# Optimization experiments

Hardware: AMD Instinct MI355X
Metric: run time of the kernel (lower is better)

## Reference

```python
import jax, jax.numpy as jnp
import numpy as np

B, T, C = 4, 2048, 1024
H = 16
HS = C // H  # 64
FF = 4 * C  # 4096


def setup_inputs() -> dict:
    key = jax.random.key(0)
    ks = jax.random.split(key, 10)
    s_in = C ** -0.5
    s_ff = FF ** -0.5
    return {
        "x": jax.random.normal(ks[0], (B, T, C), dtype=jnp.float32),
        "Wq": jax.random.normal(ks[1], (H, C, HS), dtype=jnp.float32) * s_in,
        "Wk": jax.random.normal(ks[2], (H, C, HS), dtype=jnp.float32) * s_in,
        "Wv": jax.random.normal(ks[3], (H, C, HS), dtype=jnp.float32) * s_in,
        "Wproj": jax.random.normal(ks[4], (C, C), dtype=jnp.float32) * s_in,
        "bproj": jax.random.normal(ks[5], (C,), dtype=jnp.float32) * 0.01,
        "W1": jax.random.normal(ks[6], (C, FF), dtype=jnp.float32) * s_in,
        "b1": jax.random.normal(ks[7], (FF,), dtype=jnp.float32) * 0.01,
        "W2": jax.random.normal(ks[8], (FF, C), dtype=jnp.float32) * s_ff,
        "b2": jax.random.normal(ks[9], (C,), dtype=jnp.float32) * 0.01,
    }


def reference(x, Wq, Wk, Wv, Wproj, bproj, W1, b1, W2, b2):
    b, t, c = x.shape
    # per-head projections, batched over heads: [B,H,T,HS]
    q = jnp.einsum("btc,hcd->bhtd", x, Wq)
    k = jnp.einsum("btc,hcd->bhtd", x, Wk)
    v = jnp.einsum("btc,hcd->bhtd", x, Wv)
    # NOTE: original scales by full embed dim c**-0.5, not head_size
    scores = jnp.einsum("bhtd,bhsd->bhts", q, k) * (c ** -0.5)
    causal = jnp.tril(jnp.ones((t, t), dtype=bool))
    scores = jnp.where(causal[None, None], scores, -jnp.inf)
    w = jax.nn.softmax(scores, axis=-1)
    y = jnp.einsum("bhts,bhsd->bhtd", w, v)  # [B,H,T,HS]
    y = jnp.transpose(y, (0, 2, 1, 3)).reshape(b, t, c)  # concat heads
    attn_out = y @ Wproj + bproj
    x = attn_out + x
    ff = jax.nn.relu(x @ W1 + b1) @ W2 + b2
    return ff + x
```

## Files before the change

kernel.cpp:

```cpp
#include <hip/hip_runtime.h>

typedef unsigned short u16;
typedef __attribute__((ext_vector_type(4))) float f32x4;
typedef __attribute__((ext_vector_type(8))) short bf16x8;

constexpr int kB  = 4;
constexpr int kT  = 2048;
constexpr int kC  = 1024;
constexpr int kH  = 16;
constexpr int kFF = 4096;
constexpr int kM  = kB * kT;
constexpr int k3C = 3 * kC;

__device__ __forceinline__ float b2f(u16 u) {
    union { unsigned int i; float f; } v;
    v.i = ((unsigned int)u) << 16;
    return v.f;
}
__device__ __forceinline__ u16 f2b(float f) {
    union { float f; unsigned int i; } v;
    v.f = f;
    unsigned int r = (v.i + 0x7FFFu + ((v.i >> 16) & 1u)) >> 16;
    return (u16)r;
}

__device__ __forceinline__ void lds_barrier() {
    __asm__ __volatile__("" ::: "memory");
    __builtin_amdgcn_s_waitcnt(0xC07F);
    __builtin_amdgcn_s_barrier();
    __asm__ __volatile__("" ::: "memory");
}

__global__ void cvt_f32_bf16(const float* __restrict__ in, u16* __restrict__ out, int n4)
{
    const int i = blockIdx.x * 256 + threadIdx.x;
    if (i >= n4) return;
    float4 v = *(const float4*)(in + (size_t)i * 4);
    ushort4 o;
    o.x = f2b(v.x); o.y = f2b(v.y); o.z = f2b(v.z); o.w = f2b(v.w);
    *(ushort4*)(out + (size_t)i * 4) = o;
}

__global__ void transpose_cvt(const float* __restrict__ in, int R, int Cc,
                              u16* __restrict__ out)
{
    __shared__ float t[32][33];
    const int bx = blockIdx.x * 32;
    const int by = blockIdx.y * 32;
    const int lx = threadIdx.x, ly = threadIdx.y;
    #pragma unroll
    for (int i = 0; i < 32; i += 8)
        t[ly + i][lx] = in[(size_t)(by + ly + i) * Cc + bx + lx];
    __syncthreads();
    #pragma unroll
    for (int i = 0; i < 32; i += 8)
        out[(size_t)(bx + ly + i) * R + by + lx] = f2b(t[lx][ly + i]);
}

__global__ void repack_qkv_t(const float* __restrict__ Wq, const float* __restrict__ Wk,
                             const float* __restrict__ Wv, u16* __restrict__ out)
{
    __shared__ float t[32][33];
    const int z = blockIdx.z;
    const int s = z >> 4, h = z & 15;
    const float* in = (s == 0 ? Wq : s == 1 ? Wk : Wv) + (size_t)h * (kC * 64);
    const int bx = blockIdx.x * 32;
    const int by = blockIdx.y * 32;
    const int lx = threadIdx.x, ly = threadIdx.y;
    #pragma unroll
    for (int i = 0; i < 32; i += 8)
        t[ly + i][lx] = in[(size_t)(by + ly + i) * 64 + bx + lx];
    __syncthreads();
    const int orow = s * kC + h * 64 + bx;
    #pragma unroll
    for (int i = 0; i < 32; i += 8)
        out[(size_t)(orow + ly + i) * kC + by + lx] = f2b(t[lx][ly + i]);
}

__global__ __launch_bounds__(256) void gemm_bt_mfma(
    const u16* __restrict__ A, int lda,
    const u16* __restrict__ Bt, int ldb,
    int K,
    const float* __restrict__ bias,
    const u16* __restrict__ resid,
    float* __restrict__ CoF,
    u16* __restrict__ CoB,
    int ldc, int do_relu)
{
    constexpr int BK = 64;
    __shared__ u16 As[128 * BK];
    __shared__ u16 Bs[128 * BK];
    const int tid  = threadIdx.x;
    const int wave = tid >> 6, lane = tid & 63;
    const int wm = (wave >> 1) * 64, wn = (wave & 1) * 64;
    const int m0 = blockIdx.y * 128, n0 = blockIdx.x * 128;

    const int srow = wave * 32;
    const int lrow = lane >> 3;
    const int scol = ((lane & 7) ^ lrow) * 8;

    const int fm   = lane & 15;
    const int fkq  = lane >> 4;

    f32x4 acc[4][4];
    #pragma unroll
    for (int i = 0; i < 4; ++i)
        #pragma unroll
        for (int j = 0; j < 4; ++j)
            acc[i][j] = (f32x4){0.f, 0.f, 0.f, 0.f};

    for (int k0 = 0; k0 < K; k0 += BK) {
        #pragma unroll
        for (int i = 0; i < 4; ++i) {
            const int r = srow + i * 8;
            const u16* ga = A  + (size_t)(m0 + r + lrow) * lda + k0 + scol;
            const u16* gb = Bt + (size_t)(n0 + r + lrow) * ldb + k0 + scol;
            __builtin_amdgcn_global_load_lds(
                (const __attribute__((address_space(1))) void*)ga,
                (__attribute__((address_space(3))) void*)&As[r * BK], 16, 0, 0);
            __builtin_amdgcn_global_load_lds(
                (const __attribute__((address_space(1))) void*)gb,
                (__attribute__((address_space(3))) void*)&Bs[r * BK], 16, 0, 0);
        }
        __syncthreads();
        #pragma unroll
        for (int ks = 0; ks < 2; ++ks) {
            bf16x8 a[4], b[4];
            #pragma unroll
            for (int i = 0; i < 4; ++i) {
                const int m = wm + i * 16 + fm;
                const int ck = ((ks * 4 + fkq) ^ (m & 7)) * 8;
                a[i] = *(const bf16x8*)&As[m * BK + ck];
            }
            #pragma unroll
            for (int j = 0; j < 4; ++j) {
                const int n = wn + j * 16 + fm;
                const int ck = ((ks * 4 + fkq) ^ (n & 7)) * 8;
                b[j] = *(const bf16x8*)&Bs[n * BK + ck];
            }
            #pragma unroll
            for (int i = 0; i < 4; ++i)
                #pragma unroll
                for (int j = 0; j < 4; ++j)
                    acc[i][j] = __builtin_amdgcn_mfma_f32_16x16x32_bf16(
                        a[i], b[j], acc[i][j], 0, 0, 0);
        }
        __syncthreads();
    }

    const int col = lane & 15;
    const int rb  = (lane >> 4) * 4;
    #pragma unroll
    for (int i = 0; i < 4; ++i) {
        #pragma unroll
        for (int j = 0; j < 4; ++j) {
            const int n = n0 + wn + j * 16 + col;
            #pragma unroll
            for (int r = 0; r < 4; ++r) {
                const int m = m0 + wm + i * 16 + rb + r;
                float v = acc[i][j][r];
                if (bias)    v += bias[n];
                if (do_relu) v = fmaxf(v, 0.f);
                if (resid)   v += b2f(resid[(size_t)m * ldc + n]);
                if (CoF) CoF[(size_t)m * ldc + n] = v;
                else     CoB[(size_t)m * ldc + n] = f2b(v);
            }
        }
    }
}

__global__ __launch_bounds__(256) void attn_mfma3(
    const u16* __restrict__ QKV, u16* __restrict__ Y)
{
    __shared__ __align__(16) u16 Kl[2][64 * 64];
    __shared__ __align__(16) u16 Vt[2][64 * 64];
    __shared__ __align__(16) u16 Pl[4][16 * 64];

    const int tid  = threadIdx.x;
    const int wave = tid >> 6, lane = tid & 63;
    const int ln = lane & 15, quad = lane >> 4;
    const int idx = blockIdx.x;
    const int bh = idx & 63;
    const int qt = 15 - (idx >> 6);
    const int b = bh >> 4, h = bh & 15;
    const int q0 = qt << 7;
    const int bT = b * kT;
    const int qgw = q0 + wave * 32;
    const float scale = 0.03125f;

    const u16* kvbase = QKV + (size_t)bT * k3C + kC + h * 64;

    const int sK = tid >> 3, cK = tid & 7;
    const int sV = (tid >> 3) * 2, cV = tid & 7;
    const int kwa0 = (sK << 6) + ((cK ^ (sK & 7)) << 3);
    const int kwa1 = kwa0 + (32 << 6);

    bf16x8 qa[2][2];
    #pragma unroll
    for (int qsub = 0; qsub < 2; ++qsub) {
        const size_t qb = ((size_t)bT + qgw + 16 * qsub + ln) * k3C + h * 64;
        qa[qsub][0] = *(const bf16x8*)(QKV + qb + quad * 8);
        qa[qsub][1] = *(const bf16x8*)(QKV + qb + 32 + quad * 8);
    }

    f32x4 acco[2][4];
    #pragma unroll
    for (int qsub = 0; qsub < 2; ++qsub)
        #pragma unroll
        for (int jd = 0; jd < 4; ++jd) acco[qsub][jd] = (f32x4){0.f, 0.f, 0.f, 0.f};
    float mrun[2] = {-1e30f, -1e30f}, lrun[2] = {0.f, 0.f};
    u16* Pw = Pl[wave];

    const int ntiles = 2 * qt + 2;

    auto loadkv = [&](int s0p, uint4& k0, uint4& k1, uint4& v0, uint4& v1) {
        const u16* kg = kvbase + (size_t)(s0p + sK) * k3C + cK * 8;
        k0 = *(const uint4*)kg;
        k1 = *(const uint4*)(kg + (size_t)32 * k3C);
        const u16* vg = kvbase + kC + (size_t)(s0p + sV) * k3C + cV * 8;
        v0 = *(const uint4*)vg;
        v1 = *(const uint4*)(vg + k3C);
    };
    auto stage = [&](u16* Kb, u16* Vb, const uint4& k0, const uint4& k1,
                     const uint4& v0, const uint4& v1) {
        *(uint4*)&Kb[kwa0] = k0;
        *(uint4*)&Kb[kwa1] = k1;
        const u16* t0 = (const u16*)&v0;
        const u16* t1 = (const u16*)&v1;
        #pragma unroll
        for (int i = 0; i < 8; ++i) {
            const int d = cV * 8 + i;
            const int chunk = ((sV >> 3) ^ (d & 7) ^ ((d >> 3) & 7)) & 7;
            ushort2 pr; pr.x = t0[i]; pr.y = t1[i];
            *(ushort2*)&Vb[(d << 6) + (chunk << 3) + (sV & 7)] = pr;
        }
    };
    auto compute = [&](int t, const u16* Kb, const u16* Vb) {
        const int s0 = t << 6;
        if (s0 > qgw + 31) return;
        f32x4 accs[2][4];
        #pragma unroll
        for (int qsub = 0; qsub < 2; ++qsub)
            #pragma unroll
            for (int j = 0; j < 4; ++j) accs[qsub][j] = (f32x4){0.f, 0.f, 0.f, 0.f};
        #pragma unroll
        for (int ks = 0; ks < 2; ++ks) {
            #pragma unroll
            for (int j = 0; j < 4; ++j) {
                const int s = j * 16 + ln;
                bf16x8 kb = *(const bf16x8*)&Kb[(s << 6) + ((((quad + 4 * ks) ^ (s & 7)) & 7) << 3)];
                accs[0][j] = __builtin_amdgcn_mfma_f32_16x16x32_bf16(kb, qa[0][ks], accs[0][j], 0, 0, 0);
                accs[1][j] = __builtin_amdgcn_mfma_f32_16x16x32_bf16(kb, qa[1][ks], accs[1][j], 0, 0, 0);
            }
        }
        bf16x8 vfr[4][2];
        #pragma unroll
        for (int jd = 0; jd < 4; ++jd) {
            const int d = jd * 16 + ln;
            #pragma unroll
            for (int ks = 0; ks < 2; ++ks)
                vfr[jd][ks] = *(const bf16x8*)&Vb[(d << 6) + ((((quad + 4 * ks) ^ (d & 7) ^ ((d >> 3) & 7)) & 7) << 3)];
        }
        #pragma unroll
        for (int qsub = 0; qsub < 2; ++qsub) {
            const int qg = qgw + 16 * qsub + ln;
            float part = -1e30f;
            #pragma unroll
            for (int j = 0; j < 4; ++j) {
                #pragma unroll
                for (int r = 0; r < 4; ++r) {
                    const int sg = s0 + j * 16 + quad * 4 + r;
                    float v = accs[qsub][j][r] * scale;
                    v = (sg <= qg) ? v : -1e30f;
                    accs[qsub][j][r] = v;
                    part = fmaxf(part, v);
                }
            }
            float mx = fmaxf(part, __shfl_xor(part, 16));
            mx = fmaxf(mx, __shfl_xor(mx, 32));
            const float mn = fmaxf(mrun[qsub], mx);
            const float al = __expf(mrun[qsub] - mn);
            mrun[qsub] = mn;
            float ls = 0.f;
            #pragma unroll
            for (int j = 0; j < 4; ++j)
                #pragma unroll
                for (int r = 0; r < 4; ++r) {
                    const float p = __expf(accs[qsub][j][r] - mn);
                    accs[qsub][j][r] = p;
                    ls += p;
                }
            ls += __shfl_xor(ls, 16);
            ls += __shfl_xor(ls, 32);
            lrun[qsub] = lrun[qsub] * al + ls;
            #pragma unroll
            for (int jd = 0; jd < 4; ++jd)
                #pragma unroll
                for (int r = 0; r < 4; ++r)
                    acco[qsub][jd][r] *= al;
            #pragma unroll
            for (int j = 0; j < 4; ++j) {
                ushort4 pk;
                pk.x = f2b(accs[qsub][j][0]); pk.y = f2b(accs[qsub][j][1]);
                pk.z = f2b(accs[qsub][j][2]); pk.w = f2b(accs[qsub][j][3]);
                const int chunk = ((2 * j + (quad >> 1)) ^ (ln & 7)) & 7;
                *(ushort4*)&Pw[(ln << 6) + (chunk << 3) + ((quad & 1) << 2)] = pk;
            }
            #pragma unroll
            for (int ks = 0; ks < 2; ++ks) {
                bf16x8 pb = *(const bf16x8*)&Pw[(ln << 6) + ((((4 * ks + quad) ^ (ln & 7)) & 7) << 3)];
                #pragma unroll
                for (int jd = 0; jd < 4; ++jd)
                    acco[qsub][jd] = __builtin_amdgcn_mfma_f32_16x16x32_bf16(
                        vfr[jd][ks], pb, acco[qsub][jd], 0, 0, 0);
            }
        }
    };

    uint4 ka0, ka1, va0, va1, kb0, kb1, vb0, vb1;
    loadkv(0, ka0, ka1, va0, va1);
    for (int t = 0; t < ntiles; t += 2) {
        stage(Kl[0], Vt[0], ka0, ka1, va0, va1);
        loadkv((t + 1) << 6, kb0, kb1, vb0, vb1);
        lds_barrier();
        compute(t, Kl[0], Vt[0]);
        stage(Kl[1], Vt[1], kb0, kb1, vb0, vb1);
        loadkv(((t + 2) < ntiles ? (t + 2) : 0) << 6, ka0, ka1, va0, va1);
        lds_barrier();
        compute(t + 1, Kl[1], Vt[1]);
    }

    #pragma unroll
    for (int qsub = 0; qsub < 2; ++qsub) {
        const float inv = 1.f / lrun[qsub];
        const size_t yrow = ((size_t)bT + qgw + 16 * qsub + ln) * kC + h * 64;
        #pragma unroll
        for (int jd = 0; jd < 4; ++jd) {
            ushort4 ov;
            ov.x = f2b(acco[qsub][jd][0] * inv);
            ov.y = f2b(acco[qsub][jd][1] * inv);
            ov.z = f2b(acco[qsub][jd][2] * inv);
            ov.w = f2b(acco[qsub][jd][3] * inv);
            *(ushort4*)(Y + yrow + jd * 16 + quad * 4) = ov;
        }
    }
}

extern "C" void kernel_launch(void* const* d_in, const int* in_sizes, int n_in,
                              void* d_out, int out_size, void* d_ws, size_t ws_size,
                              hipStream_t stream) {
    const float* x     = (const float*)d_in[0];
    const float* Wq    = (const float*)d_in[1];
    const float* Wk    = (const float*)d_in[2];
    const float* Wv    = (const float*)d_in[3];
    const float* Wproj = (const float*)d_in[4];
    const float* bproj = (const float*)d_in[5];
    const float* W1    = (const float*)d_in[6];
    const float* b1    = (const float*)d_in[7];
    const float* W2    = (const float*)d_in[8];
    const float* b2    = (const float*)d_in[9];

    u16* ws      = (u16*)d_ws;
    u16* QKV     = ws;
    u16* ffh     = ws;
    u16* attn_y  = ws + (size_t)kM * kFF;
    u16* xb      = attn_y  + (size_t)kM * kC;
    u16* res1    = xb      + (size_t)kM * kC;
    u16* Wqkv_t  = res1    + (size_t)kM * kC;
    u16* Wproj_t = Wqkv_t  + (size_t)k3C * kC;
    u16* W1t     = Wproj_t + (size_t)kC * kC;
    u16* W2t     = W1t     + (size_t)kFF * kC;
    float* out   = (float*)d_out;

    cvt_f32_bf16<<<(kM * kC / 4 + 255) / 256, 256, 0, stream>>>(x, xb, kM * kC / 4);
    repack_qkv_t<<<dim3(2, kC / 32, 48), dim3(32, 8), 0, stream>>>(Wq, Wk, Wv, Wqkv_t);
    transpose_cvt<<<dim3(kC / 32, kC / 32),  dim3(32, 8), 0, stream>>>(Wproj, kC, kC, Wproj_t);
    transpose_cvt<<<dim3(kFF / 32, kC / 32), dim3(32, 8), 0, stream>>>(W1, kC, kFF, W1t);
    transpose_cvt<<<dim3(kC / 32, kFF / 32), dim3(32, 8), 0, stream>>>(W2, kFF, kC, W2t);

    gemm_bt_mfma<<<dim3(k3C / 128, kM / 128), 256, 0, stream>>>(
        xb, kC, Wqkv_t, kC, kC, nullptr, nullptr, nullptr, QKV, k3C, 0);
    attn_mfma3<<<dim3(1024), 256, 0, stream>>>(QKV, attn_y);
    gemm_bt_mfma<<<dim3(kC / 128, kM / 128), 256, 0, stream>>>(
        attn_y, kC, Wproj_t, kC, kC, bproj, xb, nullptr, res1, kC, 0);
    gemm_bt_mfma<<<dim3(kFF / 128, kM / 128), 256, 0, stream>>>(
        res1, kC, W1t, kC, kC, b1, nullptr, nullptr, ffh, kFF, 1);
    gemm_bt_mfma<<<dim3(kC / 128, kM / 128), 256, 0, stream>>>(
        ffh, kFF, W2t, kFF, kFF, b2, res1, out, nullptr, kC, 0);
}
```

Measured before the change: 588.0 us.

## Replace GEMM with 256x256 double-buffered ping-pong pipelined MFMA kernel

Measured after the change: 649.4 us. +10.4%, slower.

```diff
diff --git a/kernel.cpp b/kernel.cpp
--- a/kernel.cpp
+++ b/kernel.cpp
@@ -29,6 +29,13 @@
     __builtin_amdgcn_s_waitcnt(0xC07F);
     __builtin_amdgcn_s_barrier();
     __asm__ __volatile__("" ::: "memory");
+}
+
+__device__ __forceinline__ void phase_barrier() {
+    __asm__ __volatile__("" ::: "memory");
+    __builtin_amdgcn_s_barrier();
+    __asm__ __volatile__("" ::: "memory");
+    __builtin_amdgcn_sched_barrier(0);
 }
 
 __global__ void cvt_f32_bf16(const float* __restrict__ in, u16* __restrict__ out, int n4)
@@ -77,7 +84,7 @@
         out[(size_t)(orow + ly + i) * kC + by + lx] = f2b(t[lx][ly + i]);
 }
 
-__global__ __launch_bounds__(256) void gemm_bt_mfma(
+__global__ __launch_bounds__(512, 2) void gemm_bt_256(
     const u16* __restrict__ A, int lda,
     const u16* __restrict__ Bt, int ldb,
     int K,
@@ -85,79 +92,130 @@
     const u16* __restrict__ resid,
     float* __restrict__ CoF,
     u16* __restrict__ CoB,
-    int ldc, int do_relu)
+    int ldc, int do_relu, int nbx)
 {
-    constexpr int BK = 64;
-    __shared__ u16 As[128 * BK];
-    __shared__ u16 Bs[128 * BK];
+    __shared__ u16 As[2][256 * 64];
+    __shared__ u16 Bs[2][256 * 64];
+
     const int tid  = threadIdx.x;
     const int wave = tid >> 6, lane = tid & 63;
-    const int wm = (wave >> 1) * 64, wn = (wave & 1) * 64;
-    const int m0 = blockIdx.y * 128, n0 = blockIdx.x * 128;
-
-    const int srow = wave * 32;
+    const int wm = wave >> 2, wn = wave & 3;
+
+    const int cpx = gridDim.x >> 3;
+    const int swz = (blockIdx.x & 7) * cpx + (blockIdx.x >> 3);
+    const int bx = swz % nbx, by = swz / nbx;
+    const int m0 = by * 256, n0 = bx * 256;
+
     const int lrow = lane >> 3;
     const int scol = ((lane & 7) ^ lrow) * 8;
-
-    const int fm   = lane & 15;
-    const int fkq  = lane >> 4;
-
-    f32x4 acc[4][4];
-    #pragma unroll
-    for (int i = 0; i < 4; ++i)
+    const int srow = wave * 8 + lrow;
+
+    const int fm = lane & 15, fkq = lane >> 4;
+
+    f32x4 acc[8][4];
+    #pragma unroll
+    for (int i = 0; i < 8; ++i)
         #pragma unroll
         for (int j = 0; j < 4; ++j)
             acc[i][j] = (f32x4){0.f, 0.f, 0.f, 0.f};
 
-    for (int k0 = 0; k0 < K; k0 += BK) {
+    const int NT = K >> 6;
+
+    auto stg = [&](const u16* g, int ld, int r0, u16* l) {
+        __builtin_amdgcn_global_load_lds(
+            (const __attribute__((address_space(1))) void*)(g + (size_t)(r0 + srow) * ld + scol),
+            (__attribute__((address_space(3))) void*)(l + (r0 + wave * 8) * 64), 16, 0, 0);
+    };
+    auto stageA = [&](int kt) {
+        const u16* g = A + (size_t)m0 * lda + kt * 64;
+        u16* l = As[kt & 1];
+        stg(g, lda, 0, l); stg(g, lda, 64, l); stg(g, lda, 128, l); stg(g, lda, 192, l);
+    };
+    auto stageBh = [&](int kt, int h) {
+        const u16* g = Bt + (size_t)n0 * ldb + kt * 64;
+        u16* l = Bs[kt & 1];
+        stg(g, ldb, h * 128, l); stg(g, ldb, h * 128 + 64, l);
+    };
+
+    bf16x8 alo[4][2], ahi[4][2], b0f[2][2], b1f[2][2];
+    auto rdA = [&](bf16x8 (&a)[4][2], const u16* S, int qm) {
         #pragma unroll
         for (int i = 0; i < 4; ++i) {
-            const int r = srow + i * 8;
-            const u16* ga = A  + (size_t)(m0 + r + lrow) * lda + k0 + scol;
-            const u16* gb = Bt + (size_t)(n0 + r + lrow) * ldb + k0 + scol;
-            __builtin_amdgcn_global_load_lds(
-                (const __attribute__((address_space(1))) void*)ga,
-                (__attribute__((address_space(3))) void*)&As[r * BK], 16, 0, 0);
-            __builtin_amdgcn_global_load_lds(
-                (const __attribute__((address_space(1))) void*)gb,
-                (__attribute__((address_space(3))) void*)&Bs[r * BK], 16, 0, 0);
-        }
-        __syncthreads();
-        #pragma unroll
-        for (int ks = 0; ks < 2; ++ks) {
-            bf16x8 a[4], b[4];
-            #pragma unroll
-            for (int i = 0; i < 4; ++i) {
-                const int m = wm + i * 16 + fm;
-                const int ck = ((ks * 4 + fkq) ^ (m & 7)) * 8;
-                a[i] = *(const bf16x8*)&As[m * BK + ck];
-            }
-            #pragma unroll
-            for (int j = 0; j < 4; ++j) {
-                const int n = wn + j * 16 + fm;
-                const int ck = ((ks * 4 + fkq) ^ (n & 7)) * 8;
-                b[j] = *(const bf16x8*)&Bs[n * BK + ck];
-            }
+            const int m = wm * 128 + qm * 64 + i * 16 + fm;
+            #pragma unroll
+            for (int ks = 0; ks < 2; ++ks)
+                a[i][ks] = *(const bf16x8*)&S[m * 64 + (((ks * 4 + fkq) ^ (fm & 7)) << 3)];
+        }
+    };
+    auto rdB = [&](bf16x8 (&b)[2][2], const u16* S, int qn) {
+        #pragma unroll
+        for (int j = 0; j < 2; ++j) {
+            const int n = wn * 64 + qn * 32 + j * 16 + fm;
+            #pragma unroll
+            for (int ks = 0; ks < 2; ++ks)
+                b[j][ks] = *(const bf16x8*)&S[n * 64 + (((ks * 4 + fkq) ^ (fm & 7)) << 3)];
+        }
+    };
+    auto mm8 = [&](bf16x8 (&a)[4][2], bf16x8 (&b)[2][2], int i0, int j0) {
+        __builtin_amdgcn_s_setprio(1);
+        #pragma unroll
+        for (int ks = 0; ks < 2; ++ks)
             #pragma unroll
             for (int i = 0; i < 4; ++i)
                 #pragma unroll
-                for (int j = 0; j < 4; ++j)
-                    acc[i][j] = __builtin_amdgcn_mfma_f32_16x16x32_bf16(
-                        a[i], b[j], acc[i][j], 0, 0, 0);
-        }
-        __syncthreads();
-    }
-
-    const int col = lane & 15;
-    const int rb  = (lane >> 4) * 4;
-    #pragma unroll
-    for (int i = 0; i < 4; ++i) {
+                for (int j = 0; j < 2; ++j)
+                    acc[i0 + i][j0 + j] = __builtin_amdgcn_mfma_f32_16x16x32_bf16(
+                        a[i][ks], b[j][ks], acc[i0 + i][j0 + j], 0, 0, 0);
+        __builtin_amdgcn_s_setprio(0);
+    };
+
+    stageA(0);
+    stageBh(0, 0); stageBh(0, 1);
+    if (NT > 1) {
+        stageA(1);
+        __asm__ __volatile__("s_waitcnt vmcnt(4)" ::: "memory");
+    } else {
+        __asm__ __volatile__("s_waitcnt vmcnt(0)" ::: "memory");
+    }
+    phase_barrier();
+
+    for (int t = 0; t < NT; ++t) {
+        const u16* Sa = As[t & 1];
+        const u16* Sb = Bs[t & 1];
+        rdA(alo, Sa, 0);
+        rdB(b0f, Sb, 0);
+        if (t + 1 < NT) stageBh(t + 1, 0);
+        phase_barrier();
+        mm8(alo, b0f, 0, 0);
+        phase_barrier();
+        rdB(b1f, Sb, 1);
+        if (t + 1 < NT) stageBh(t + 1, 1);
+        phase_barrier();
+        mm8(alo, b1f, 0, 2);
+        phase_barrier();
+        rdA(ahi, Sa, 1);
+        phase_barrier();
+        mm8(ahi, b1f, 4, 2);
+        phase_barrier();
+        if (t + 2 < NT) stageA(t + 2);
+        phase_barrier();
+        mm8(ahi, b0f, 4, 0);
+        if (t + 1 < NT) {
+            if (t + 2 < NT) { __asm__ __volatile__("s_waitcnt vmcnt(4)" ::: "memory"); }
+            else            { __asm__ __volatile__("s_waitcnt vmcnt(0)" ::: "memory"); }
+        }
+        phase_barrier();
+    }
+
+    #pragma unroll
+    for (int i = 0; i < 8; ++i) {
+        const int mb = m0 + wm * 128 + i * 16 + (lane >> 4) * 4;
         #pragma unroll
         for (int j = 0; j < 4; ++j) {
-            const int n = n0 + wn + j * 16 + col;
+            const int n = n0 + wn * 64 + j * 16 + (lane & 15);
             #pragma unroll
             for (int r = 0; r < 4; ++r) {
-                const int m = m0 + wm + i * 16 + rb + r;
+                const int m = mb + r;
                 float v = acc[i][j][r];
                 if (bias)    v += bias[n];
                 if (do_relu) v = fmaxf(v, 0.f);
@@ -378,13 +436,13 @@
     transpose_cvt<<<dim3(kFF / 32, kC / 32), dim3(32, 8), 0, stream>>>(W1, kC, kFF, W1t);
     transpose_cvt<<<dim3(kC / 32, kFF / 32), dim3(32, 8), 0, stream>>>(W2, kFF, kC, W2t);
 
-    gemm_bt_mfma<<<dim3(k3C / 128, kM / 128), 256, 0, stream>>>(
-        xb, kC, Wqkv_t, kC, kC, nullptr, nullptr, nullptr, QKV, k3C, 0);
+    gemm_bt_256<<<dim3((k3C / 256) * (kM / 256)), 512, 0, stream>>>(
+        xb, kC, Wqkv_t, kC, kC, nullptr, nullptr, nullptr, QKV, k3C, 0, k3C / 256);
     attn_mfma3<<<dim3(1024), 256, 0, stream>>>(QKV, attn_y);
-    gemm_bt_mfma<<<dim3(kC / 128, kM / 128), 256, 0, stream>>>(
-        attn_y, kC, Wproj_t, kC, kC, bproj, xb, nullptr, res1, kC, 0);
-    gemm_bt_mfma<<<dim3(kFF / 128, kM / 128), 256, 0, stream>>>(
-        res1, kC, W1t, kC, kC, b1, nullptr, nullptr, ffh, kFF, 1);
-    gemm_bt_mfma<<<dim3(kC / 128, kM / 128), 256, 0, stream>>>(
-        ffh, kFF, W2t, kFF, kFF, b2, res1, out, nullptr, kC, 0);
-}
+    gemm_bt_256<<<dim3((kC / 256) * (kM / 256)), 512, 0, stream>>>(
+        attn_y, kC, Wproj_t, kC, kC, bproj, xb, nullptr, res1, kC, 0, kC / 256);
+    gemm_bt_256<<<dim3((kFF / 256) * (kM / 256)), 512, 0, stream>>>(
+        res1, kC, W1t, kC, kC, b1, nullptr, nullptr, ffh, kFF, 1, kFF / 256);
+    gemm_bt_256<<<dim3((kC / 256) * (kM / 256)), 512, 0, stream>>>(
+        ffh, kFF, W2t, kFF, kFF, b2, res1, out, nullptr, kC, 0, kC / 256);
+}
```

## Double-buffer GEMM LDS tiles with 256x128 blocks and swizzled block order

Applied to the files above, without the earlier changes.

New measurement: 590.9 us. Within noise of the previous version (+0.5%).

```diff
diff --git a/kernel.cpp b/kernel.cpp
--- a/kernel.cpp
+++ b/kernel.cpp
@@ -29,6 +29,13 @@
     __builtin_amdgcn_s_waitcnt(0xC07F);
     __builtin_amdgcn_s_barrier();
     __asm__ __volatile__("" ::: "memory");
+}
+
+__device__ __forceinline__ void tile_barrier() {
+    __builtin_amdgcn_sched_barrier(0);
+    __asm__ __volatile__("s_waitcnt vmcnt(0)" ::: "memory");
+    __builtin_amdgcn_s_barrier();
+    __builtin_amdgcn_sched_barrier(0);
 }
 
 __global__ void cvt_f32_bf16(const float* __restrict__ in, u16* __restrict__ out, int n4)
@@ -77,7 +84,7 @@
         out[(size_t)(orow + ly + i) * kC + by + lx] = f2b(t[lx][ly + i]);
 }
 
-__global__ __launch_bounds__(256) void gemm_bt_mfma(
+__global__ __launch_bounds__(512, 2) void gemm_bt_2ph(
     const u16* __restrict__ A, int lda,
     const u16* __restrict__ Bt, int ldb,
     int K,
@@ -85,22 +92,24 @@
     const u16* __restrict__ resid,
     float* __restrict__ CoF,
     u16* __restrict__ CoB,
-    int ldc, int do_relu)
+    int ldc, int do_relu, int nbx)
 {
-    constexpr int BK = 64;
-    __shared__ u16 As[128 * BK];
-    __shared__ u16 Bs[128 * BK];
+    __shared__ u16 As[2][256 * 64];
+    __shared__ u16 Bs[2][128 * 64];
+
     const int tid  = threadIdx.x;
     const int wave = tid >> 6, lane = tid & 63;
     const int wm = (wave >> 1) * 64, wn = (wave & 1) * 64;
-    const int m0 = blockIdx.y * 128, n0 = blockIdx.x * 128;
-
-    const int srow = wave * 32;
+
+    const int cpx = gridDim.x >> 3;
+    const int swz = (blockIdx.x & 7) * cpx + (blockIdx.x >> 3);
+    const int bx = swz % nbx, by = swz / nbx;
+    const int m0 = by * 256, n0 = bx * 128;
+
     const int lrow = lane >> 3;
     const int scol = ((lane & 7) ^ lrow) * 8;
 
-    const int fm   = lane & 15;
-    const int fkq  = lane >> 4;
+    const int fm = lane & 15, fkq = lane >> 4;
 
     f32x4 acc[4][4];
     #pragma unroll
@@ -109,34 +118,42 @@
         for (int j = 0; j < 4; ++j)
             acc[i][j] = (f32x4){0.f, 0.f, 0.f, 0.f};
 
-    for (int k0 = 0; k0 < K; k0 += BK) {
-        #pragma unroll
-        for (int i = 0; i < 4; ++i) {
-            const int r = srow + i * 8;
-            const u16* ga = A  + (size_t)(m0 + r + lrow) * lda + k0 + scol;
-            const u16* gb = Bt + (size_t)(n0 + r + lrow) * ldb + k0 + scol;
-            __builtin_amdgcn_global_load_lds(
-                (const __attribute__((address_space(1))) void*)ga,
-                (__attribute__((address_space(3))) void*)&As[r * BK], 16, 0, 0);
-            __builtin_amdgcn_global_load_lds(
-                (const __attribute__((address_space(1))) void*)gb,
-                (__attribute__((address_space(3))) void*)&Bs[r * BK], 16, 0, 0);
-        }
-        __syncthreads();
+    const int NT = K >> 6;
+
+    auto stg = [&](const u16* g, int ld, int r0, u16* l) {
+        __builtin_amdgcn_global_load_lds(
+            (const __attribute__((address_space(1))) void*)(g + (size_t)(r0 + wave * 8 + lrow) * ld + scol),
+            (__attribute__((address_space(3))) void*)(l + (r0 + wave * 8) * 64), 16, 0, 0);
+    };
+    auto stageAB = [&](int kt) {
+        const u16* ga = A  + (size_t)m0 * lda + kt * 64;
+        const u16* gb = Bt + (size_t)n0 * ldb + kt * 64;
+        u16* la = As[kt & 1];
+        u16* lb = Bs[kt & 1];
+        stg(ga, lda, 0, la);   stg(ga, lda, 64, la);
+        stg(ga, lda, 128, la); stg(ga, lda, 192, la);
+        stg(gb, ldb, 0, lb);   stg(gb, ldb, 64, lb);
+    };
+
+    stageAB(0);
+    tile_barrier();
+
+    for (int t = 0; t < NT; ++t) {
+        if (t + 1 < NT) stageAB(t + 1);
+        const u16* Sa = As[t & 1];
+        const u16* Sb = Bs[t & 1];
         #pragma unroll
         for (int ks = 0; ks < 2; ++ks) {
             bf16x8 a[4], b[4];
             #pragma unroll
             for (int i = 0; i < 4; ++i) {
                 const int m = wm + i * 16 + fm;
-                const int ck = ((ks * 4 + fkq) ^ (m & 7)) * 8;
-                a[i] = *(const bf16x8*)&As[m * BK + ck];
+                a[i] = *(const bf16x8*)&Sa[m * 64 + (((ks * 4 + fkq) ^ (fm & 7)) << 3)];
             }
             #pragma unroll
             for (int j = 0; j < 4; ++j) {
                 const int n = wn + j * 16 + fm;
-                const int ck = ((ks * 4 + fkq) ^ (n & 7)) * 8;
-                b[j] = *(const bf16x8*)&Bs[n * BK + ck];
+                b[j] = *(const bf16x8*)&Sb[n * 64 + (((ks * 4 + fkq) ^ (fm & 7)) << 3)];
             }
             #pragma unroll
             for (int i = 0; i < 4; ++i)
@@ -145,7 +162,7 @@
                     acc[i][j] = __builtin_amdgcn_mfma_f32_16x16x32_bf16(
                         a[i], b[j], acc[i][j], 0, 0, 0);
         }
-        __syncthreads();
+        if (t + 1 < NT) tile_barrier();
     }
 
     const int col = lane & 15;
@@ -378,13 +395,13 @@
     transpose_cvt<<<dim3(kFF / 32, kC / 32), dim3(32, 8), 0, stream>>>(W1, kC, kFF, W1t);
     transpose_cvt<<<dim3(kC / 32, kFF / 32), dim3(32, 8), 0, stream>>>(W2, kFF, kC, W2t);
 
-    gemm_bt_mfma<<<dim3(k3C / 128, kM / 128), 256, 0, stream>>>(
-        xb, kC, Wqkv_t, kC, kC, nullptr, nullptr, nullptr, QKV, k3C, 0);
+    gemm_bt_2ph<<<dim3((kM / 256) * (k3C / 128)), 512, 0, stream>>>(
+        xb, kC, Wqkv_t, kC, kC, nullptr, nullptr, nullptr, QKV, k3C, 0, k3C / 128);
     attn_mfma3<<<dim3(1024), 256, 0, stream>>>(QKV, attn_y);
-    gemm_bt_mfma<<<dim3(kC / 128, kM / 128), 256, 0, stream>>>(
-        attn_y, kC, Wproj_t, kC, kC, bproj, xb, nullptr, res1, kC, 0);
-    gemm_bt_mfma<<<dim3(kFF / 128, kM / 128), 256, 0, stream>>>(
-        res1, kC, W1t, kC, kC, b1, nullptr, nullptr, ffh, kFF, 1);
-    gemm_bt_mfma<<<dim3(kC / 128, kM / 128), 256, 0, stream>>>(
-        ffh, kFF, W2t, kFF, kFF, b2, res1, out, nullptr, kC, 0);
-}
+    gemm_bt_2ph<<<dim3((kM / 256) * (kC / 128)), 512, 0, stream>>>(
+        attn_y, kC, Wproj_t, kC, kC, bproj, xb, nullptr, res1, kC, 0, kC / 128);
+    gemm_bt_2ph<<<dim3((kM / 256) * (kFF / 128)), 512, 0, stream>>>(
+        res1, kC, W1t, kC, kC, b1, nullptr, nullptr, ffh, kFF, 1, kFF / 128);
+    gemm_bt_2ph<<<dim3((kM / 256) * (kC / 128)), 512, 0, stream>>>(
+        ffh, kFF, W2t, kFF, kFF, b2, res1, out, nullptr, kC, 0, kC / 128);
+}
```
